# Kernel tuning notes

Measured on AMD Instinct MI355X. Metric: run time of the kernel, lower is better.

The kernel has to match this reference:

```python
import jax, jax.numpy as jnp
import numpy as np

N, C, NUM_GROUPS = 4_194_304, 16, 8


def setup_inputs() -> dict:
    key = jax.random.key(0)
    k1, k2, k3 = jax.random.split(key, 3)
    input_ = jax.random.normal(k1, (N, C), dtype=jnp.float32)
    target = jax.random.randint(k2, (N,), 0, C, dtype=jnp.int64) if jax.config.jax_enable_x64 else jax.random.randint(k2, (N,), 0, C, dtype=jnp.int32)
    group = jax.random.randint(k3, (N,), 0, NUM_GROUPS, dtype=jnp.int32)
    return {"input_": input_, "target": target, "group": group}


def reference(input_, target, group):
    # gather input_[i, target[i]] and take |1 - .|
    err = jnp.abs(1.0 - jnp.take_along_axis(input_, target[:, None].astype(jnp.int32), axis=1)[:, 0])  # [N]
    # per-group mean == L1-row-normalized one-hot matmul in the original
    sums = jax.ops.segment_sum(err, group, num_segments=NUM_GROUPS)               # [G]
    counts = jax.ops.segment_sum(jnp.ones_like(err), group, num_segments=NUM_GROUPS)
    means = jnp.where(counts > 0, sums / jnp.maximum(counts, 1.0), 0.0)           # empty group -> 0 (F.normalize eps behavior)
    loss_target_value = 0.5
    return jnp.abs(loss_target_value - means.mean())
```

## Files before the change

### kernel.cpp

```cpp
#include <hip/hip_runtime.h>

#define N_ELEMS 4194304
#define C_DIM 16
#define G_NUM 8
#define ROWS_PER_STAGE 256
#define NUM_STAGES (N_ELEMS / ROWS_PER_STAGE)


__global__ __launch_bounds__(256) void berl_partial(
    const float* __restrict__ input_,
    const int*   __restrict__ target,
    const int*   __restrict__ group,
    float*        __restrict__ g_sums,
    unsigned int* __restrict__ g_counts)
{
    __shared__ float4       s_rows[ROWS_PER_STAGE * 4];
    __shared__ float        s_sums[G_NUM];
    __shared__ unsigned int s_counts[G_NUM];

    const int tid = threadIdx.x;
    if (tid < G_NUM) { s_sums[tid] = 0.0f; s_counts[tid] = 0u; }

    float sums[G_NUM];
    float cnts[G_NUM];
#pragma unroll
    for (int k = 0; k < G_NUM; ++k) { sums[k] = 0.0f; cnts[k] = 0.0f; }

    const float4* __restrict__ in4 = (const float4*)input_;

    for (int s = blockIdx.x; s < NUM_STAGES; s += gridDim.x) {
        const int row0 = s * ROWS_PER_STAGE;
        const int f4_base = row0 * 4;

#pragma unroll
        for (int q = 0; q < 4; ++q) {
            s_rows[tid + 256 * q] = in4[f4_base + tid + 256 * q];
        }
        __syncthreads();

        const int t = target[row0 + tid];
        const int g = group[row0 + tid];
        const float v = ((const float*)s_rows)[tid * C_DIM + t];
        const float e = fabsf(1.0f - v);
#pragma unroll
        for (int k = 0; k < G_NUM; ++k) {
            sums[k] += (g == k) ? e : 0.0f;
            cnts[k] += (g == k) ? 1.0f : 0.0f;
        }
        __syncthreads();
    }

#pragma unroll
    for (int k = 0; k < G_NUM; ++k) {
        atomicAdd(&s_sums[k], sums[k]);
        atomicAdd(&s_counts[k], (unsigned int)cnts[k]);
    }
    __syncthreads();

    if (tid < G_NUM) {
        atomicAdd(&g_sums[tid], s_sums[tid]);
        atomicAdd(&g_counts[tid], s_counts[tid]);
    }
}

__global__ void berl_final(const float* __restrict__ g_sums,
                           const unsigned int* __restrict__ g_counts,
                           float* __restrict__ out)
{
    if (threadIdx.x == 0 && blockIdx.x == 0) {
        float acc = 0.0f;
#pragma unroll
        for (int g = 0; g < G_NUM; ++g) {
            float c = (float)g_counts[g];
            float m = (c > 0.0f) ? (g_sums[g] / fmaxf(c, 1.0f)) : 0.0f;
            acc += m;
        }
        out[0] = fabsf(0.5f - acc / (float)G_NUM);
    }
}

extern "C" void kernel_launch(void* const* d_in, const int* in_sizes, int n_in,
                              void* d_out, int out_size, void* d_ws, size_t ws_size,
                              hipStream_t stream) {
    const float* input_ = (const float*)d_in[0];
    const int*   target = (const int*)d_in[1];
    const int*   group  = (const int*)d_in[2];
    float* out = (float*)d_out;

    float*        g_sums   = (float*)d_ws;
    unsigned int* g_counts = (unsigned int*)((char*)d_ws + G_NUM * sizeof(float));

    hipMemsetAsync(d_ws, 0, G_NUM * (sizeof(float) + sizeof(unsigned int)), stream);

    dim3 block(256);
    dim3 grid(2048);
    berl_partial<<<grid, block, 0, stream>>>(input_, target, group, g_sums, g_counts);
    berl_final<<<1, 64, 0, stream>>>(g_sums, g_counts, out);
}
```

Baseline: 446.5 us.

## Stream input as nontemporal float4 loads without shared-memory staging

Drops the shared-memory staging and the two barriers per stage. Each thread now does grid-strided nontemporal float4 loads, unrolled four deep, and keeps only the float4 that holds the target column; the others count as zero contributions. This targets barrier stalls and the LDS round-trip, and puts more loads in flight. The cost is four redundant target/group loads per row, though they should hit in cache.

```diff
diff --git a/kernel.cpp b/kernel.cpp
--- a/kernel.cpp
+++ b/kernel.cpp
@@ -3,21 +3,43 @@
 #define N_ELEMS 4194304
 #define C_DIM 16
 #define G_NUM 8
-#define ROWS_PER_STAGE 256
-#define NUM_STAGES (N_ELEMS / ROWS_PER_STAGE)
+
+#define THREADS 256
+#define GRID 2048
+#define NF4 (N_ELEMS * (C_DIM / 4))
+#define ITERS (NF4 / (GRID * THREADS))
+#define UNROLL 4
+
+typedef float vfloat4 __attribute__((ext_vector_type(4)));
 
 
-__global__ __launch_bounds__(256) void berl_partial(
+__device__ __forceinline__ void process_one(vfloat4 v, int j, int t, int g,
+                                            float* sums, float* cnts)
+{
+    const int f  = j & 3;
+    const int tf = t >> 2;
+    const int c  = t & 3;
+    float x = (c == 0) ? v.x : (c == 1) ? v.y : (c == 2) ? v.z : v.w;
+    const bool hit = (f == tf);
+    const float e   = hit ? fabsf(1.0f - x) : 0.0f;
+    const float one = hit ? 1.0f : 0.0f;
+#pragma unroll
+    for (int k = 0; k < G_NUM; ++k) {
+        const bool m = (g == k);
+        sums[k] += m ? e : 0.0f;
+        cnts[k] += m ? one : 0.0f;
+    }
+}
+
+__global__ __launch_bounds__(THREADS) void berl_partial(
     const float* __restrict__ input_,
     const int*   __restrict__ target,
     const int*   __restrict__ group,
     float*        __restrict__ g_sums,
     unsigned int* __restrict__ g_counts)
 {
-    __shared__ float4       s_rows[ROWS_PER_STAGE * 4];
     __shared__ float        s_sums[G_NUM];
     __shared__ unsigned int s_counts[G_NUM];
-
     const int tid = threadIdx.x;
     if (tid < G_NUM) { s_sums[tid] = 0.0f; s_counts[tid] = 0u; }
 
@@ -26,30 +48,33 @@
 #pragma unroll
     for (int k = 0; k < G_NUM; ++k) { sums[k] = 0.0f; cnts[k] = 0.0f; }
 
-    const float4* __restrict__ in4 = (const float4*)input_;
+    const vfloat4* __restrict__ in4 = (const vfloat4*)input_;
+    const int base   = blockIdx.x * THREADS + tid;
+    const int stride = GRID * THREADS;
 
-    for (int s = blockIdx.x; s < NUM_STAGES; s += gridDim.x) {
-        const int row0 = s * ROWS_PER_STAGE;
-        const int f4_base = row0 * 4;
-
+#pragma unroll 1
+    for (int it = 0; it < ITERS; it += UNROLL) {
+        int     j[UNROLL];
+        vfloat4 v[UNROLL];
+        int     t[UNROLL], g[UNROLL];
 #pragma unroll
-        for (int q = 0; q < 4; ++q) {
-            s_rows[tid + 256 * q] = in4[f4_base + tid + 256 * q];
+        for (int u = 0; u < UNROLL; ++u) {
+            j[u] = base + (it + u) * stride;
+            v[u] = __builtin_nontemporal_load(&in4[j[u]]);
         }
-        __syncthreads();
-
-        const int t = target[row0 + tid];
-        const int g = group[row0 + tid];
-        const float v = ((const float*)s_rows)[tid * C_DIM + t];
-        const float e = fabsf(1.0f - v);
 #pragma unroll
-        for (int k = 0; k < G_NUM; ++k) {
-            sums[k] += (g == k) ? e : 0.0f;
-            cnts[k] += (g == k) ? 1.0f : 0.0f;
+        for (int u = 0; u < UNROLL; ++u) {
+            const int r = j[u] >> 2;
+            t[u] = target[r];
+            g[u] = group[r];
         }
-        __syncthreads();
+#pragma unroll
+        for (int u = 0; u < UNROLL; ++u) {
+            process_one(v[u], j[u], t[u], g[u], sums, cnts);
+        }
     }
 
+    __syncthreads();
 #pragma unroll
     for (int k = 0; k < G_NUM; ++k) {
         atomicAdd(&s_sums[k], sums[k]);
@@ -90,10 +115,8 @@
     float*        g_sums   = (float*)d_ws;
     unsigned int* g_counts = (unsigned int*)((char*)d_ws + G_NUM * sizeof(float));
 
-    hipMemsetAsync(d_ws, 0, G_NUM * (sizeof(float) + sizeof(unsigned int)), stream);
+    (void)hipMemsetAsync(d_ws, 0, G_NUM * (sizeof(float) + sizeof(unsigned int)), stream);
 
-    dim3 block(256);
-    dim3 grid(2048);
-    berl_partial<<<grid, block, 0, stream>>>(input_, target, group, g_sums, g_counts);
+    berl_partial<<<dim3(GRID), dim3(THREADS), 0, stream>>>(input_, target, group, g_sums, g_counts);
     berl_final<<<1, 64, 0, stream>>>(g_sums, g_counts, out);
 }
```

Measured after the change: 435.4 us. -2.5%, faster.
